# Performance work log

Hardware: AMD Instinct MI355X
Metric: run time of the kernel (lower is better)

Reference implementation:

```python
import jax, jax.numpy as jnp
import numpy as np

N, E, D, H, G, C = 100000, 1200000, 64, 64, 128, 10


def setup_inputs() -> dict:
    key = jax.random.key(0)
    ks = jax.random.split(key, 20)
    def lin(k, fin, fout):
        kw, kb = jax.random.split(k)
        s = 1.0 / np.sqrt(fin)
        return (jax.random.uniform(kw, (fin, fout), jnp.float32, -s, s),
                jax.random.uniform(kb, (fout,), jnp.float32, -s, s))
    w1a, b1a = lin(ks[0], D, H)
    w1b, b1b = lin(ks[1], H, H)
    w2a, b2a = lin(ks[2], H, H)
    w2b, b2b = lin(ks[3], H, H)
    w3a, b3a = lin(ks[4], H, H)
    w3b, b3b = lin(ks[5], H, H)
    wc, bc = lin(ks[6], H, C)
    x = jax.random.normal(ks[7], (N, D), jnp.float32)
    edge_index = jax.random.randint(ks[8], (2, E), 0, N, dtype=jnp.int32)
    batch = jnp.sort(jax.random.randint(ks[9], (N,), 0, G, dtype=jnp.int32))
    return {"x": x, "w1a": w1a, "b1a": b1a, "w1b": w1b, "b1b": b1b,
            "w2a": w2a, "b2a": b2a, "w2b": w2b, "b2b": b2b,
            "w3a": w3a, "b3a": b3a, "w3b": w3b, "b3b": b3b,
            "wc": wc, "bc": bc, "edge_index": edge_index, "batch": batch}


def _gin_layer(x, src, dst, wa, ba, wb, bb):
    # GINConv (eps=0): mlp(x + sum_{j in N(i)} x_j), then outer ReLU from GIN.forward
    agg = jax.ops.segment_sum(x[src], dst, num_segments=N)  # [N, d]
    h = x + agg
    h = jax.nn.relu(h @ wa + ba) @ wb + bb
    return jax.nn.relu(h)


def reference(x, w1a, b1a, w1b, b1b, w2a, b2a, w2b, b2b,
              w3a, b3a, w3b, b3b, wc, bc, edge_index, batch):
    src, dst = edge_index[0], edge_index[1]
    x = _gin_layer(x, src, dst, w1a, b1a, w1b, b1b)
    x = _gin_layer(x, src, dst, w2a, b2a, w2b, b2b)
    x = _gin_layer(x, src, dst, w3a, b3a, w3b, b3b)
    # global mean pool over graphs
    sums = jax.ops.segment_sum(x, batch, num_segments=G)              # [G, H]
    cnts = jax.ops.segment_sum(jnp.ones((N,), x.dtype), batch, num_segments=G)
    pooled = sums / jnp.maximum(cnts, 1.0)[:, None]
    return pooled @ wc + bc  # [G, C]
```

## Files before the change

kernel.cpp:

```cpp
#include <hip/hip_runtime.h>
#include <hip/hip_bf16.h>


#define N_NODES 100000
#define N_EDGES 1200000
#define N_GRAPH 128
#define N_CLS   10
#define NBUCK   391
#define BCAP    4096
#define BSH     12
#define HALFN   50000

typedef __bf16 bf16_t;
typedef __bf16 bf16x8 __attribute__((ext_vector_type(8)));
typedef float  f32x4  __attribute__((ext_vector_type(4)));

__global__ void tobf_kernel(const float* __restrict__ x, bf16_t* __restrict__ xb,
                            int* __restrict__ bcnt, float* __restrict__ gsum) {
    if (blockIdx.x == 0) {
        for (int i = threadIdx.x; i < NBUCK; i += 256) bcnt[i] = 0;
    } else if (blockIdx.x == 1) {
        f32x4* g4 = (f32x4*)gsum;
        for (int i = threadIdx.x; i < N_GRAPH * 16; i += 256)
            g4[i] = (f32x4){0.f, 0.f, 0.f, 0.f};
    }
    const int i = (blockIdx.x * 256 + threadIdx.x) * 8;
    const f32x4 a = *(const f32x4*)(x + i);
    const f32x4 b = *(const f32x4*)(x + i + 4);
    bf16x8 o;
#pragma unroll
    for (int j = 0; j < 4; ++j) { o[j] = (bf16_t)a[j]; o[4 + j] = (bf16_t)b[j]; }
    *(bf16x8*)(xb + i) = o;
}

__global__ void binA_kernel(const int* __restrict__ ei,
                            int* __restrict__ bcnt,
                            int* __restrict__ bpair) {
    __shared__ int lcnt[NBUCK];
    __shared__ int lbase[NBUCK];
    const int t = threadIdx.x;
    for (int b = t; b < NBUCK; b += 256) lcnt[b] = 0;
    __syncthreads();
    const int e0 = (blockIdx.x * 256 + t) * 4;
    int4 s4, d4; int b[4], r[4];
    const bool valid = e0 < N_EDGES;
    if (valid) {
        s4 = *(const int4*)(ei + e0);
        d4 = *(const int4*)(ei + N_EDGES + e0);
        b[0] = d4.x >> 8; b[1] = d4.y >> 8; b[2] = d4.z >> 8; b[3] = d4.w >> 8;
        r[0] = atomicAdd(&lcnt[b[0]], 1);
        r[1] = atomicAdd(&lcnt[b[1]], 1);
        r[2] = atomicAdd(&lcnt[b[2]], 1);
        r[3] = atomicAdd(&lcnt[b[3]], 1);
    }
    __syncthreads();
    for (int bb = t; bb < NBUCK; bb += 256) {
        const int c = lcnt[bb];
        lbase[bb] = c ? atomicAdd(&bcnt[bb], c) : 0;
    }
    __syncthreads();
    if (valid) {
        const int ss[4] = {s4.x, s4.y, s4.z, s4.w};
        const int dd[4] = {d4.x, d4.y, d4.z, d4.w};
#pragma unroll
        for (int j = 0; j < 4; ++j) {
            const int slot = lbase[b[j]] + r[j];
            if (slot < BCAP)
                bpair[(b[j] << BSH) + slot] = (ss[j] << 8) | (dd[j] & 255);
        }
    }
}

__global__ void sortfill_kernel(const int* __restrict__ bpair,
                                const int* __restrict__ bcnt,
                                int* __restrict__ offset, int* __restrict__ csr) {
    __shared__ int red[256];
    __shared__ int hist[256];
    __shared__ int l[256];
    __shared__ int cursor[256];
    const int b = blockIdx.x;
    const int t = threadIdx.x;
    const int base = b << BSH;

    int part = 0;
    for (int i = t; i < b; i += 256) {
        int c = bcnt[i];
        part += (c < BCAP ? c : BCAP);
    }
    red[t] = part;
    __syncthreads();
    for (int d = 128; d > 0; d >>= 1) {
        if (t < d) red[t] += red[t + d];
        __syncthreads();
    }
    const int cbase = red[0];
    int cnt = bcnt[b];
    cnt = cnt < BCAP ? cnt : BCAP;
    if (b == NBUCK - 1 && t == 0) offset[N_NODES] = cbase + cnt;
    __syncthreads();

    hist[t] = 0;
    __syncthreads();
    for (int i = t; i < cnt; i += 256)
        atomicAdd(&hist[bpair[base + i] & 255], 1);
    __syncthreads();

    const int v = hist[t];
    l[t] = v;
    __syncthreads();
    for (int d = 1; d < 256; d <<= 1) {
        int u = l[t];
        if (t >= d) u += l[t - d];
        __syncthreads();
        l[t] = u;
        __syncthreads();
    }
    const int gpos = cbase + l[t] - v;
    const int node = (b << 8) + t;
    if (node < N_NODES) offset[node] = gpos;
    cursor[t] = gpos;
    __syncthreads();

    for (int i = t; i < cnt; i += 256) {
        const int p = bpair[base + i];
        const int pos = atomicAdd(&cursor[p & 255], 1);
        csr[pos] = p >> 8;
    }
}

#define GATHER8(S, ACC)                                                        \
    {                                                                          \
        const int t0 = __shfl(S, j + 0), t1 = __shfl(S, j + 1);                \
        const int t2 = __shfl(S, j + 2), t3 = __shfl(S, j + 3);                \
        const int t4 = __shfl(S, j + 4), t5 = __shfl(S, j + 5);                \
        const int t6 = __shfl(S, j + 6), t7 = __shfl(S, j + 7);                \
        const float u0 = (float)x[t0 * 64 + f], u1 = (float)x[t1 * 64 + f];    \
        const float u2 = (float)x[t2 * 64 + f], u3 = (float)x[t3 * 64 + f];    \
        const float u4 = (float)x[t4 * 64 + f], u5 = (float)x[t5 * 64 + f];    \
        const float u6 = (float)x[t6 * 64 + f], u7 = (float)x[t7 * 64 + f];    \
        ACC += ((u0 + u1) + (u2 + u3)) + ((u4 + u5) + (u6 + u7));              \
    }
#define GATHER4(S, J, ACC)                                                     \
    {                                                                          \
        const int t0 = __shfl(S, J + 0), t1 = __shfl(S, J + 1);                \
        const int t2 = __shfl(S, J + 2), t3 = __shfl(S, J + 3);                \
        const float u0 = (float)x[t0 * 64 + f], u1 = (float)x[t1 * 64 + f];    \
        const float u2 = (float)x[t2 * 64 + f], u3 = (float)x[t3 * 64 + f];    \
        ACC += (u0 + u1) + (u2 + u3);                                          \
    }

__global__ void agg2_kernel(const bf16_t* __restrict__ x,
                            const int* __restrict__ offset,
                            const int* __restrict__ csr,
                            bf16_t* __restrict__ hout) {
    const int w = (blockIdx.x * 256 + threadIdx.x) >> 6;
    const int f = threadIdx.x & 63;
    const int nA = w;
    const int nB = w + HALFN;

    const int oA = offset[nA], eA = offset[nA + 1];
    const int oB = offset[nB], eB = offset[nB + 1];
    const int dA = eA - oA, dB = eB - oB;

    float accA = (float)x[nA * 64 + f];
    float accB = (float)x[nB * 64 + f];

    for (int base = 0; base < dA || base < dB; base += 64) {
        const int ra = dA - base, rb2 = dB - base;
        const int cntA = ra <= 0 ? 0 : (ra < 64 ? ra : 64);
        const int cntB = rb2 <= 0 ? 0 : (rb2 < 64 ? rb2 : 64);
        int sA = 0, sB = 0;
        if (f < cntA) sA = csr[oA + base + f];
        if (f < cntB) sB = csr[oB + base + f];

        int j = 0;
        for (; j + 8 <= cntA && j + 8 <= cntB; j += 8) {
            GATHER8(sA, accA)
            GATHER8(sB, accB)
        }
        int jA = j, jB = j;
        for (; jA + 8 <= cntA; jA += 8) { const int j = jA; GATHER8(sA, accA) }
        for (; jB + 8 <= cntB; jB += 8) { const int j = jB; GATHER8(sB, accB) }
        if (jA + 4 <= cntA && jB + 4 <= cntB) {
            GATHER4(sA, jA, accA)
            GATHER4(sB, jB, accB)
            jA += 4; jB += 4;
        }
        if (jA + 4 <= cntA) { GATHER4(sA, jA, accA) jA += 4; }
        if (jB + 4 <= cntB) { GATHER4(sB, jB, accB) jB += 4; }
        for (; jA < cntA; ++jA) { const int t = __shfl(sA, jA); accA += (float)x[t * 64 + f]; }
        for (; jB < cntB; ++jB) { const int t = __shfl(sB, jB); accB += (float)x[t * 64 + f]; }
    }
    hout[nA * 64 + f] = (bf16_t)accA;
    hout[nB * 64 + f] = (bf16_t)accB;
}

template <int POOL>
__global__ void mlp_kernel(const bf16_t* __restrict__ hin,
                           const float* __restrict__ wa, const float* __restrict__ ba,
                           const float* __restrict__ wb, const float* __restrict__ bb,
                           bf16_t* __restrict__ xout,
                           const int* __restrict__ batch,
                           float* __restrict__ gsum) {
    __shared__ __align__(16) bf16_t wfrag[2][8][64][8];
    __shared__ __align__(16) bf16_t hs[4][16][72];
    __shared__ float biasA[64], biasB[64];

    const int tid  = threadIdx.x;
    const int wv   = tid >> 6;
    const int lane = tid & 63;
    const int l15  = lane & 15;
    const int quad = lane >> 4;

    {
        const int k  = tid >> 2;
        const int n0 = (tid & 3) << 4;
        const int ks = k >> 5, qd = (k >> 3) & 3, jj = k & 7;
        const int fi = ((n0 >> 4) << 1) + ks;
#pragma unroll
        for (int m = 0; m < 2; ++m) {
            const float* w = m ? wb : wa;
            const f32x4 v0 = *(const f32x4*)(w + k * 64 + n0);
            const f32x4 v1 = *(const f32x4*)(w + k * 64 + n0 + 4);
            const f32x4 v2 = *(const f32x4*)(w + k * 64 + n0 + 8);
            const f32x4 v3 = *(const f32x4*)(w + k * 64 + n0 + 12);
#pragma unroll
            for (int l = 0; l < 4; ++l) {
                wfrag[m][fi][qd * 16 + l][jj]      = (bf16_t)v0[l];
                wfrag[m][fi][qd * 16 + 4 + l][jj]  = (bf16_t)v1[l];
                wfrag[m][fi][qd * 16 + 8 + l][jj]  = (bf16_t)v2[l];
                wfrag[m][fi][qd * 16 + 12 + l][jj] = (bf16_t)v3[l];
            }
        }
        if (tid < 64) biasA[tid] = ba[tid];
        else if (tid < 128) biasB[tid - 64] = bb[tid - 64];
    }
    __syncthreads();

    const int ntiles = (N_NODES + 63) / 64;
    int tile = blockIdx.x;

    bf16x8 af[2];
    {
        const int rowa = tile * 64 + wv * 16 + l15;
        const int rowc = rowa < N_NODES ? rowa : N_NODES - 1;
#pragma unroll
        for (int ks = 0; ks < 2; ++ks)
            af[ks] = *(const bf16x8*)(hin + rowc * 64 + ks * 32 + quad * 8);
    }

    for (;;) {
        const int next = tile + gridDim.x;
        const bool has_next = next < ntiles;

        bf16x8 afn[2];
        if (has_next) {
            const int rowa = next * 64 + wv * 16 + l15;
            const int rowc = rowa < N_NODES ? rowa : N_NODES - 1;
#pragma unroll
            for (int ks = 0; ks < 2; ++ks)
                afn[ks] = *(const bf16x8*)(hin + rowc * 64 + ks * 32 + quad * 8);
        }

        const int rb = tile * 64 + wv * 16;

#pragma unroll
        for (int ct = 0; ct < 4; ++ct) {
            const bf16x8 b0 = *(const bf16x8*)&wfrag[0][ct * 2 + 0][lane][0];
            const bf16x8 b1 = *(const bf16x8*)&wfrag[0][ct * 2 + 1][lane][0];
            f32x4 acc = {0.f, 0.f, 0.f, 0.f};
            acc = __builtin_amdgcn_mfma_f32_16x16x32_bf16(af[0], b0, acc, 0, 0, 0);
            acc = __builtin_amdgcn_mfma_f32_16x16x32_bf16(af[1], b1, acc, 0, 0, 0);
            const float bv = biasA[ct * 16 + l15];
#pragma unroll
            for (int r = 0; r < 4; ++r) {
                float h = acc[r] + bv;
                h = h > 0.f ? h : 0.f;
                hs[wv][quad * 4 + r][ct * 16 + l15] = (bf16_t)h;
            }
        }

        bf16x8 a2[2];
#pragma unroll
        for (int ks = 0; ks < 2; ++ks)
            a2[ks] = *(const bf16x8*)(&hs[wv][l15][ks * 32 + quad * 8]);

#pragma unroll
        for (int ct = 0; ct < 4; ++ct) {
            const bf16x8 b0 = *(const bf16x8*)&wfrag[1][ct * 2 + 0][lane][0];
            const bf16x8 b1 = *(const bf16x8*)&wfrag[1][ct * 2 + 1][lane][0];
            f32x4 acc = {0.f, 0.f, 0.f, 0.f};
            acc = __builtin_amdgcn_mfma_f32_16x16x32_bf16(a2[0], b0, acc, 0, 0, 0);
            acc = __builtin_amdgcn_mfma_f32_16x16x32_bf16(a2[1], b1, acc, 0, 0, 0);
            const float bv = biasB[ct * 16 + l15];
#pragma unroll
            for (int r = 0; r < 4; ++r) {
                float h = acc[r] + bv;
                h = h > 0.f ? h : 0.f;
                hs[wv][quad * 4 + r][ct * 16 + l15] = (bf16_t)h;
            }
        }

        if (POOL) {
            int cur = -1;
            float acc = 0.f;
            for (int r = 0; r < 16; ++r) {
                const int row = rb + r;
                if (row >= N_NODES) break;
                const int g = batch[row];
                const float v = (float)hs[wv][r][lane];
                if (g != cur) {
                    if (cur >= 0) unsafeAtomicAdd(gsum + cur * 64 + lane, acc);
                    acc = 0.f;
                    cur = g;
                }
                acc += v;
            }
            if (cur >= 0) unsafeAtomicAdd(gsum + cur * 64 + lane, acc);
        } else {
            const int colg = (lane & 7) * 8;
#pragma unroll
            for (int sx = 0; sx < 2; ++sx) {
                const int r16 = (lane >> 3) + 8 * sx;
                const int grow = rb + r16;
                const bf16x8 v = *(const bf16x8*)&hs[wv][r16][colg];
                if (grow < N_NODES)
                    *(bf16x8*)(xout + grow * 64 + colg) = v;
            }
        }

        if (!has_next) break;
        af[0] = afn[0];
        af[1] = afn[1];
        tile = next;
    }
}

__global__ void cls_kernel(const float* __restrict__ gsum,
                           const int* __restrict__ batch,
                           const float* __restrict__ wc, const float* __restrict__ bc,
                           float* __restrict__ out) {
    const int g = blockIdx.x;
    const int c = threadIdx.x;
    if (c >= N_CLS) return;
    int lo = 0, hi = N_NODES;
    while (lo < hi) { const int m = (lo + hi) >> 1; if (batch[m] < g) lo = m + 1; else hi = m; }
    const int lb = lo;
    lo = 0; hi = N_NODES;
    while (lo < hi) { const int m = (lo + hi) >> 1; if (batch[m] <= g) lo = m + 1; else hi = m; }
    const int cnt = lo - lb;
    const float inv = 1.f / (float)(cnt > 1 ? cnt : 1);
    float acc = bc[c];
    for (int k = 0; k < 64; ++k)
        acc += gsum[g * 64 + k] * inv * wc[k * N_CLS + c];
    out[g * N_CLS + c] = acc;
}

extern "C" void kernel_launch(void* const* d_in, const int* in_sizes, int n_in,
                              void* d_out, int out_size, void* d_ws, size_t ws_size,
                              hipStream_t stream) {
    const float* x   = (const float*)d_in[0];
    const float* w1a = (const float*)d_in[1];
    const float* b1a = (const float*)d_in[2];
    const float* w1b = (const float*)d_in[3];
    const float* b1b = (const float*)d_in[4];
    const float* w2a = (const float*)d_in[5];
    const float* b2a = (const float*)d_in[6];
    const float* w2b = (const float*)d_in[7];
    const float* b2b = (const float*)d_in[8];
    const float* w3a = (const float*)d_in[9];
    const float* b3a = (const float*)d_in[10];
    const float* w3b = (const float*)d_in[11];
    const float* b3b = (const float*)d_in[12];
    const float* wc  = (const float*)d_in[13];
    const float* bc  = (const float*)d_in[14];
    const int*   ei    = (const int*)d_in[15];
    const int*   batch = (const int*)d_in[16];
    float* out = (float*)d_out;

    char*   ws     = (char*)d_ws;
    int*    bcnt   = (int*)ws;
    int*    offset = (int*)(ws + 3136);
    int*    csr    = (int*)(ws + 403152);
    int*    bpair  = (int*)(ws + 5203152);
    bf16_t* xbf    = (bf16_t*)(ws + 11609296);
    bf16_t* h      = (bf16_t*)(ws + 24409296);
    bf16_t* xA     = (bf16_t*)(ws + 37209296);
    float*  gsum   = (float*)(ws + 50009296);

    const int e4grid  = (N_EDGES / 4 + 255) / 256;
    const int a2grid  = HALFN / 4;
    const int mlpgrid = 782;

    tobf_kernel<<<(N_NODES * 64) / (256 * 8), 256, 0, stream>>>(x, xbf, bcnt, gsum);

    binA_kernel<<<e4grid, 256, 0, stream>>>(ei, bcnt, bpair);
    sortfill_kernel<<<NBUCK, 256, 0, stream>>>(bpair, bcnt, offset, csr);

    agg2_kernel<<<a2grid, 256, 0, stream>>>(xbf, offset, csr, h);
    mlp_kernel<0><<<mlpgrid, 256, 0, stream>>>(h, w1a, b1a, w1b, b1b, xA, nullptr, nullptr);
    agg2_kernel<<<a2grid, 256, 0, stream>>>(xA, offset, csr, h);
    mlp_kernel<0><<<mlpgrid, 256, 0, stream>>>(h, w2a, b2a, w2b, b2b, xA, nullptr, nullptr);
    agg2_kernel<<<a2grid, 256, 0, stream>>>(xA, offset, csr, h);
    mlp_kernel<1><<<mlpgrid, 256, 0, stream>>>(h, w3a, b3a, w3b, b3b, nullptr, batch, gsum);

    cls_kernel<<<N_GRAPH, 64, 0, stream>>>(gsum, batch, wc, bc, out);
}
```

Before: 323.7 us.

## Fuse neighbor aggregation into the MLP kernel per 64-node tile

Merges the separate gather/aggregation kernel and the two-layer MLP kernel into one kernel. Each wavefront aggregates its 16 nodes into shared memory and then runs the MFMA MLP on them directly. This removes the bf16 round trip of the aggregated features through global memory and cuts three kernel launches. In exchange, each block now reloads and converts the weights into shared memory, the grid is one block per tile instead of a persistent loop, and the gather loop runs sequentially over 8 node pairs per wave, which may lower memory-level parallelism. Ping-pong buffers are swapped so the input and output of each layer never alias.

```diff
diff --git a/kernel.cpp b/kernel.cpp
--- a/kernel.cpp
+++ b/kernel.cpp
@@ -9,7 +9,6 @@
 #define NBUCK   391
 #define BCAP    4096
 #define BSH     12
-#define HALFN   50000
 
 typedef __bf16 bf16_t;
 typedef __bf16 bf16x8 __attribute__((ext_vector_type(8)));
@@ -149,59 +148,15 @@
         ACC += (u0 + u1) + (u2 + u3);                                          \
     }
 
-__global__ void agg2_kernel(const bf16_t* __restrict__ x,
+template <int POOL>
+__global__ void gmlp_kernel(const bf16_t* __restrict__ x,
                             const int* __restrict__ offset,
                             const int* __restrict__ csr,
-                            bf16_t* __restrict__ hout) {
-    const int w = (blockIdx.x * 256 + threadIdx.x) >> 6;
-    const int f = threadIdx.x & 63;
-    const int nA = w;
-    const int nB = w + HALFN;
-
-    const int oA = offset[nA], eA = offset[nA + 1];
-    const int oB = offset[nB], eB = offset[nB + 1];
-    const int dA = eA - oA, dB = eB - oB;
-
-    float accA = (float)x[nA * 64 + f];
-    float accB = (float)x[nB * 64 + f];
-
-    for (int base = 0; base < dA || base < dB; base += 64) {
-        const int ra = dA - base, rb2 = dB - base;
-        const int cntA = ra <= 0 ? 0 : (ra < 64 ? ra : 64);
-        const int cntB = rb2 <= 0 ? 0 : (rb2 < 64 ? rb2 : 64);
-        int sA = 0, sB = 0;
-        if (f < cntA) sA = csr[oA + base + f];
-        if (f < cntB) sB = csr[oB + base + f];
-
-        int j = 0;
-        for (; j + 8 <= cntA && j + 8 <= cntB; j += 8) {
-            GATHER8(sA, accA)
-            GATHER8(sB, accB)
-        }
-        int jA = j, jB = j;
-        for (; jA + 8 <= cntA; jA += 8) { const int j = jA; GATHER8(sA, accA) }
-        for (; jB + 8 <= cntB; jB += 8) { const int j = jB; GATHER8(sB, accB) }
-        if (jA + 4 <= cntA && jB + 4 <= cntB) {
-            GATHER4(sA, jA, accA)
-            GATHER4(sB, jB, accB)
-            jA += 4; jB += 4;
-        }
-        if (jA + 4 <= cntA) { GATHER4(sA, jA, accA) jA += 4; }
-        if (jB + 4 <= cntB) { GATHER4(sB, jB, accB) jB += 4; }
-        for (; jA < cntA; ++jA) { const int t = __shfl(sA, jA); accA += (float)x[t * 64 + f]; }
-        for (; jB < cntB; ++jB) { const int t = __shfl(sB, jB); accB += (float)x[t * 64 + f]; }
-    }
-    hout[nA * 64 + f] = (bf16_t)accA;
-    hout[nB * 64 + f] = (bf16_t)accB;
-}
-
-template <int POOL>
-__global__ void mlp_kernel(const bf16_t* __restrict__ hin,
-                           const float* __restrict__ wa, const float* __restrict__ ba,
-                           const float* __restrict__ wb, const float* __restrict__ bb,
-                           bf16_t* __restrict__ xout,
-                           const int* __restrict__ batch,
-                           float* __restrict__ gsum) {
+                            const float* __restrict__ wa, const float* __restrict__ ba,
+                            const float* __restrict__ wb, const float* __restrict__ bb,
+                            bf16_t* __restrict__ xout,
+                            const int* __restrict__ batch,
+                            float* __restrict__ gsum) {
     __shared__ __align__(16) bf16_t wfrag[2][8][64][8];
     __shared__ __align__(16) bf16_t hs[4][16][72];
     __shared__ float biasA[64], biasB[64];
@@ -237,102 +192,121 @@
     }
     __syncthreads();
 
-    const int ntiles = (N_NODES + 63) / 64;
-    int tile = blockIdx.x;
+    const int rb = blockIdx.x * 64 + wv * 16;
+    const int f  = lane;
+
+    for (int i = 0; i < 8; ++i) {
+        const int nA = rb + i;
+        const int nB = rb + i + 8;
+        const bool vA = nA < N_NODES;
+        const bool vB = nB < N_NODES;
+        const int oA = vA ? offset[nA] : 0;
+        const int eA = vA ? offset[nA + 1] : 0;
+        const int oB = vB ? offset[nB] : 0;
+        const int eB = vB ? offset[nB + 1] : 0;
+        const int dA = eA - oA, dB = eB - oB;
+
+        float accA = vA ? (float)x[nA * 64 + f] : 0.f;
+        float accB = vB ? (float)x[nB * 64 + f] : 0.f;
+
+        for (int base = 0; base < dA || base < dB; base += 64) {
+            const int ra = dA - base, rb2 = dB - base;
+            const int cntA = ra <= 0 ? 0 : (ra < 64 ? ra : 64);
+            const int cntB = rb2 <= 0 ? 0 : (rb2 < 64 ? rb2 : 64);
+            int sA = 0, sB = 0;
+            if (f < cntA) sA = csr[oA + base + f];
+            if (f < cntB) sB = csr[oB + base + f];
+
+            int j = 0;
+            for (; j + 8 <= cntA && j + 8 <= cntB; j += 8) {
+                GATHER8(sA, accA)
+                GATHER8(sB, accB)
+            }
+            int jA = j, jB = j;
+            for (; jA + 8 <= cntA; jA += 8) { const int j = jA; GATHER8(sA, accA) }
+            for (; jB + 8 <= cntB; jB += 8) { const int j = jB; GATHER8(sB, accB) }
+            if (jA + 4 <= cntA && jB + 4 <= cntB) {
+                GATHER4(sA, jA, accA)
+                GATHER4(sB, jB, accB)
+                jA += 4; jB += 4;
+            }
+            if (jA + 4 <= cntA) { GATHER4(sA, jA, accA) jA += 4; }
+            if (jB + 4 <= cntB) { GATHER4(sB, jB, accB) jB += 4; }
+            for (; jA < cntA; ++jA) { const int t = __shfl(sA, jA); accA += (float)x[t * 64 + f]; }
+            for (; jB < cntB; ++jB) { const int t = __shfl(sB, jB); accB += (float)x[t * 64 + f]; }
+        }
+        hs[wv][i][lane]     = (bf16_t)accA;
+        hs[wv][i + 8][lane] = (bf16_t)accB;
+    }
 
     bf16x8 af[2];
-    {
-        const int rowa = tile * 64 + wv * 16 + l15;
-        const int rowc = rowa < N_NODES ? rowa : N_NODES - 1;
-#pragma unroll
-        for (int ks = 0; ks < 2; ++ks)
-            af[ks] = *(const bf16x8*)(hin + rowc * 64 + ks * 32 + quad * 8);
-    }
-
-    for (;;) {
-        const int next = tile + gridDim.x;
-        const bool has_next = next < ntiles;
-
-        bf16x8 afn[2];
-        if (has_next) {
-            const int rowa = next * 64 + wv * 16 + l15;
-            const int rowc = rowa < N_NODES ? rowa : N_NODES - 1;
-#pragma unroll
-            for (int ks = 0; ks < 2; ++ks)
-                afn[ks] = *(const bf16x8*)(hin + rowc * 64 + ks * 32 + quad * 8);
-        }
-
-        const int rb = tile * 64 + wv * 16;
-
-#pragma unroll
-        for (int ct = 0; ct < 4; ++ct) {
-            const bf16x8 b0 = *(const bf16x8*)&wfrag[0][ct * 2 + 0][lane][0];
-            const bf16x8 b1 = *(const bf16x8*)&wfrag[0][ct * 2 + 1][lane][0];
-            f32x4 acc = {0.f, 0.f, 0.f, 0.f};
-            acc = __builtin_amdgcn_mfma_f32_16x16x32_bf16(af[0], b0, acc, 0, 0, 0);
-            acc = __builtin_amdgcn_mfma_f32_16x16x32_bf16(af[1], b1, acc, 0, 0, 0);
-            const float bv = biasA[ct * 16 + l15];
-#pragma unroll
-            for (int r = 0; r < 4; ++r) {
-                float h = acc[r] + bv;
-                h = h > 0.f ? h : 0.f;
-                hs[wv][quad * 4 + r][ct * 16 + l15] = (bf16_t)h;
+#pragma unroll
+    for (int ks = 0; ks < 2; ++ks)
+        af[ks] = *(const bf16x8*)(&hs[wv][l15][ks * 32 + quad * 8]);
+
+#pragma unroll
+    for (int ct = 0; ct < 4; ++ct) {
+        const bf16x8 b0 = *(const bf16x8*)&wfrag[0][ct * 2 + 0][lane][0];
+        const bf16x8 b1 = *(const bf16x8*)&wfrag[0][ct * 2 + 1][lane][0];
+        f32x4 acc = {0.f, 0.f, 0.f, 0.f};
+        acc = __builtin_amdgcn_mfma_f32_16x16x32_bf16(af[0], b0, acc, 0, 0, 0);
+        acc = __builtin_amdgcn_mfma_f32_16x16x32_bf16(af[1], b1, acc, 0, 0, 0);
+        const float bv = biasA[ct * 16 + l15];
+#pragma unroll
+        for (int r = 0; r < 4; ++r) {
+            float h = acc[r] + bv;
+            h = h > 0.f ? h : 0.f;
+            hs[wv][quad * 4 + r][ct * 16 + l15] = (bf16_t)h;
+        }
+    }
+
+    bf16x8 a2[2];
+#pragma unroll
+    for (int ks = 0; ks < 2; ++ks)
+        a2[ks] = *(const bf16x8*)(&hs[wv][l15][ks * 32 + quad * 8]);
+
+#pragma unroll
+    for (int ct = 0; ct < 4; ++ct) {
+        const bf16x8 b0 = *(const bf16x8*)&wfrag[1][ct * 2 + 0][lane][0];
+        const bf16x8 b1 = *(const bf16x8*)&wfrag[1][ct * 2 + 1][lane][0];
+        f32x4 acc = {0.f, 0.f, 0.f, 0.f};
+        acc = __builtin_amdgcn_mfma_f32_16x16x32_bf16(a2[0], b0, acc, 0, 0, 0);
+        acc = __builtin_amdgcn_mfma_f32_16x16x32_bf16(a2[1], b1, acc, 0, 0, 0);
+        const float bv = biasB[ct * 16 + l15];
+#pragma unroll
+        for (int r = 0; r < 4; ++r) {
+            float h = acc[r] + bv;
+            h = h > 0.f ? h : 0.f;
+            hs[wv][quad * 4 + r][ct * 16 + l15] = (bf16_t)h;
+        }
+    }
+
+    if (POOL) {
+        int cur = -1;
+        float acc = 0.f;
+        for (int r = 0; r < 16; ++r) {
+            const int row = rb + r;
+            if (row >= N_NODES) break;
+            const int g = batch[row];
+            const float v = (float)hs[wv][r][lane];
+            if (g != cur) {
+                if (cur >= 0) unsafeAtomicAdd(gsum + cur * 64 + lane, acc);
+                acc = 0.f;
+                cur = g;
             }
-        }
-
-        bf16x8 a2[2];
-#pragma unroll
-        for (int ks = 0; ks < 2; ++ks)
-            a2[ks] = *(const bf16x8*)(&hs[wv][l15][ks * 32 + quad * 8]);
-
-#pragma unroll
-        for (int ct = 0; ct < 4; ++ct) {
-            const bf16x8 b0 = *(const bf16x8*)&wfrag[1][ct * 2 + 0][lane][0];
-            const bf16x8 b1 = *(const bf16x8*)&wfrag[1][ct * 2 + 1][lane][0];
-            f32x4 acc = {0.f, 0.f, 0.f, 0.f};
-            acc = __builtin_amdgcn_mfma_f32_16x16x32_bf16(a2[0], b0, acc, 0, 0, 0);
-            acc = __builtin_amdgcn_mfma_f32_16x16x32_bf16(a2[1], b1, acc, 0, 0, 0);
-            const float bv = biasB[ct * 16 + l15];
-#pragma unroll
-            for (int r = 0; r < 4; ++r) {
-                float h = acc[r] + bv;
-                h = h > 0.f ? h : 0.f;
-                hs[wv][quad * 4 + r][ct * 16 + l15] = (bf16_t)h;
-            }
-        }
-
-        if (POOL) {
-            int cur = -1;
-            float acc = 0.f;
-            for (int r = 0; r < 16; ++r) {
-                const int row = rb + r;
-                if (row >= N_NODES) break;
-                const int g = batch[row];
-                const float v = (float)hs[wv][r][lane];
-                if (g != cur) {
-                    if (cur >= 0) unsafeAtomicAdd(gsum + cur * 64 + lane, acc);
-                    acc = 0.f;
-                    cur = g;
-                }
-                acc += v;
-            }
-            if (cur >= 0) unsafeAtomicAdd(gsum + cur * 64 + lane, acc);
-        } else {
-            const int colg = (lane & 7) * 8;
-#pragma unroll
-            for (int sx = 0; sx < 2; ++sx) {
-                const int r16 = (lane >> 3) + 8 * sx;
-                const int grow = rb + r16;
-                const bf16x8 v = *(const bf16x8*)&hs[wv][r16][colg];
-                if (grow < N_NODES)
-                    *(bf16x8*)(xout + grow * 64 + colg) = v;
-            }
-        }
-
-        if (!has_next) break;
-        af[0] = afn[0];
-        af[1] = afn[1];
-        tile = next;
+            acc += v;
+        }
+        if (cur >= 0) unsafeAtomicAdd(gsum + cur * 64 + lane, acc);
+    } else {
+        const int colg = (lane & 7) * 8;
+#pragma unroll
+        for (int sx = 0; sx < 2; ++sx) {
+            const int r16 = (lane >> 3) + 8 * sx;
+            const int grow = rb + r16;
+            const bf16x8 v = *(const bf16x8*)&hs[wv][r16][colg];
+            if (grow < N_NODES)
+                *(bf16x8*)(xout + grow * 64 + colg) = v;
+        }
     }
 }
 
@@ -388,21 +362,17 @@
     bf16_t* xA     = (bf16_t*)(ws + 37209296);
     float*  gsum   = (float*)(ws + 50009296);
 
-    const int e4grid  = (N_EDGES / 4 + 255) / 256;
-    const int a2grid  = HALFN / 4;
-    const int mlpgrid = 782;
+    const int e4grid = (N_EDGES / 4 + 255) / 256;
+    const int tiles  = (N_NODES + 63) / 64;
 
     tobf_kernel<<<(N_NODES * 64) / (256 * 8), 256, 0, stream>>>(x, xbf, bcnt, gsum);
 
     binA_kernel<<<e4grid, 256, 0, stream>>>(ei, bcnt, bpair);
     sortfill_kernel<<<NBUCK, 256, 0, stream>>>(bpair, bcnt, offset, csr);
 
-    agg2_kernel<<<a2grid, 256, 0, stream>>>(xbf, offset, csr, h);
-    mlp_kernel<0><<<mlpgrid, 256, 0, stream>>>(h, w1a, b1a, w1b, b1b, xA, nullptr, nullptr);
-    agg2_kernel<<<a2grid, 256, 0, stream>>>(xA, offset, csr, h);
-    mlp_kernel<0><<<mlpgrid, 256, 0, stream>>>(h, w2a, b2a, w2b, b2b, xA, nullptr, nullptr);
-    agg2_kernel<<<a2grid, 256, 0, stream>>>(xA, offset, csr, h);
-    mlp_kernel<1><<<mlpgrid, 256, 0, stream>>>(h, w3a, b3a, w3b, b3b, nullptr, batch, gsum);
+    gmlp_kernel<0><<<tiles, 256, 0, stream>>>(xbf, offset, csr, w1a, b1a, w1b, b1b, xA, nullptr, nullptr);
+    gmlp_kernel<0><<<tiles, 256, 0, stream>>>(xA, offset, csr, w2a, b2a, w2b, b2b, h, nullptr, nullptr);
+    gmlp_kernel<1><<<tiles, 256, 0, stream>>>(h, offset, csr, w3a, b3a, w3b, b3b, nullptr, batch, gsum);
 
     cls_kernel<<<N_GRAPH, 64, 0, stream>>>(gsum, batch, wc, bc, out);
 }
```

Result: slower. 376.0 us (+16.2%).
